# Performance work log

Measured on AMD Instinct MI355X. Metric: run time of the kernel, lower is better.

Reference implementation:

```python
import jax, jax.numpy as jnp
import numpy as np

EPS = 1e-8          # EPSILON in source
THRESH = 0.5        # state.match_threshold
MIN_RADIUS = 0.05   # meaningful-observation threshold

B, T, H, D, N = 4, 4096, 2048, 256, 32768
Hq = H // 4


def setup_inputs() -> dict:
    key = jax.random.key(0)
    ks = jax.random.split(key, 10)
    s = 0.02
    return {
        "hidden": jax.random.normal(ks[0], (B, T, H), jnp.float32),
        "beliefs": jax.random.normal(ks[1], (N, D), jnp.float32),
        "active_mask": jax.random.bernoulli(ks[2], 0.5, (N,)),
        "W_obs": jax.random.normal(ks[3], (D, H), jnp.float32) * s,
        "W_g1": jax.random.normal(ks[4], (Hq, H), jnp.float32) * s,
        "b_g1": jnp.zeros((Hq,), jnp.float32),
        "W_g2": jax.random.normal(ks[5], (1, Hq), jnp.float32) * s,
        "b_g2": jnp.full((1,), -2.0, jnp.float32),  # nn.init.constant_(bias, -2.0)
        "W_p1": jax.random.normal(ks[6], (Hq, H), jnp.float32) * s,
        "b_p1": jnp.zeros((Hq,), jnp.float32),
        "W_p2": jax.random.normal(ks[7], (1, Hq), jnp.float32) * s,
        "b_p2": jnp.zeros((1,), jnp.float32),
    }


def reference(hidden, beliefs, active_mask, W_obs, W_g1, b_g1, W_g2, b_g2,
              W_p1, b_p1, W_p2, b_p2):
    # --- projections (torch Linear: y = x @ W.T + b) ---
    obs = jnp.einsum("bth,dh->btd", hidden, W_obs)                       # [B,T,D]
    gate = jax.nn.sigmoid(
        jnp.einsum("btq,oq->bto",
                   jax.nn.relu(jnp.einsum("bth,qh->btq", hidden, W_g1) + b_g1),
                   W_g2) + b_g2)                                          # [B,T,1]
    prec = jax.nn.softplus(
        jnp.einsum("btq,oq->bto",
                   jax.nn.relu(jnp.einsum("bth,qh->btq", hidden, W_p1) + b_p1),
                   W_p2) + b_p2)                                          # [B,T,1]
    gated_prec = gate * prec

    obs_mean = obs.mean(axis=0)          # [T,D]
    prec_mean = gated_prec.mean(axis=0)  # [T,1]
    # F.normalize: x / max(||x||, eps)
    obs_angles = obs_mean / jnp.maximum(
        jnp.linalg.norm(obs_mean, axis=-1, keepdims=True), EPS)
    obs_beliefs = obs_angles * prec_mean  # [T,D] radius = precision

    # --- cosine-similarity 1-NN match against active beliefs ---
    b_radii = jnp.clip(jnp.linalg.norm(beliefs, axis=-1), EPS, None)     # [N]
    b_angles = beliefs / b_radii[:, None]
    o_radii_c = jnp.clip(jnp.linalg.norm(obs_beliefs, axis=-1), EPS, None)
    o_angles = obs_beliefs / o_radii_c[:, None]
    sims = jnp.einsum("td,nd->tn", o_angles, b_angles)                    # [T,N]
    sims_masked = jnp.where(active_mask[None, :], sims, -jnp.inf)
    any_active = jnp.any(active_mask)
    best_sims = jnp.where(any_active, jnp.max(sims_masked, axis=-1), 0.0)  # [T]
    best_global = jnp.where(any_active, jnp.argmax(sims_masked, axis=-1), -1)

    obs_radii = jnp.linalg.norm(obs_beliefs, axis=-1)  # unclamped
    meaningful = obs_radii > MIN_RADIUS
    matched = meaningful & (best_sims > THRESH) & any_active
    slots = jnp.where(matched, best_global, -1)          # matched slot or -1 (new)
    sims_out = jnp.where(matched, best_sims, 0.0)
    return obs_beliefs, sims_out, slots, meaningful
```

## Files before the change

kernel.cpp:

```cpp
#include <hip/hip_runtime.h>
#include <hip/hip_bf16.h>
#include <math.h>

#define TB 4
#define TT 4096
#define HH 2048
#define DD 256
#define NN 32768
#define HQ 512
#define MM (TB*TT)

typedef __attribute__((ext_vector_type(8))) short bf16x8;
typedef __attribute__((ext_vector_type(8))) _Float16 f16x8;
typedef __attribute__((ext_vector_type(4))) float f32x4;

__device__ inline unsigned short f2bf(float x){
  __hip_bfloat16 h = __float2bfloat16(x);
  return *reinterpret_cast<unsigned short*>(&h);
}

__device__ inline unsigned short f2h(float x){
  _Float16 h = (_Float16)x;
  unsigned short u; __builtin_memcpy(&u, &h, 2); return u;
}

__device__ inline bf16x8 as_bf16x8(uint4 u){ bf16x8 r; __builtin_memcpy(&r,&u,16); return r; }

__device__ __forceinline__ void gload_ldsv(const void* g, void* l){
  __builtin_amdgcn_global_load_lds(
      (const __attribute__((address_space(1))) unsigned int*)g,
      (__attribute__((address_space(3))) unsigned int*)l, 16, 0, 0);
}

#define PREP_MEAN 8192
#define PREP_CVTW 1024
#define PREP_WOBS 512
#define PREP_BEL  8192
#define PREP_ZERO 129
#define PREP_GRID (PREP_MEAN+PREP_CVTW+PREP_WOBS+PREP_BEL+PREP_ZERO)
__global__ __launch_bounds__(256) void k_prep(
    const float* __restrict__ h, unsigned short* __restrict__ hmb,
    const float* __restrict__ Wg1, const float* __restrict__ Wp1,
    unsigned short* __restrict__ Wsw,
    const float* __restrict__ Wobs, unsigned short* __restrict__ wob,
    const float* __restrict__ bel, unsigned short* __restrict__ bbf,
    unsigned int* __restrict__ zbase){
  const int b = blockIdx.x;
  if (b < PREP_MEAN){
    const size_t i = (size_t)b*256 + threadIdx.x;
    const size_t TH4 = (size_t)TT*HH/4;
    const float4* p = (const float4*)h;
    float4 v0 = p[i], v1 = p[i+TH4], v2 = p[i+2*TH4], v3 = p[i+3*TH4];
    float4 m;
    m.x = 0.25f*(v0.x+v1.x+v2.x+v3.x);
    m.y = 0.25f*(v0.y+v1.y+v2.y+v3.y);
    m.z = 0.25f*(v0.z+v1.z+v2.z+v3.z);
    m.w = 0.25f*(v0.w+v1.w+v2.w+v3.w);
    ushort4 o; o.x = f2bf(m.x); o.y = f2bf(m.y); o.z = f2bf(m.z); o.w = f2bf(m.w);
    *(ushort4*)(hmb + i*4) = o;
  } else if (b < PREP_MEAN + PREP_CVTW){
    const int id = (b - PREP_MEAN)*256 + threadIdx.x;
    const int n = id >> 8;
    const int cg = id & 255;
    const int k = cg*8;
    const int kc = cg >> 2;
    const int c8 = cg & 3;
    const float* src = (n < HQ) ? (Wg1 + (size_t)n*HH + k) : (Wp1 + (size_t)(n-HQ)*HH + k);
    float4 v0 = *(const float4*)src;
    float4 v1 = *(const float4*)(src + 4);
    unsigned short o[8] = {f2h(v0.x),f2h(v0.y),f2h(v0.z),f2h(v0.w),
                           f2h(v1.x),f2h(v1.y),f2h(v1.z),f2h(v1.w)};
    const int nb = n >> 8, r = n & 255;
    const int s = (r & 3) ^ ((r >> 2) & 3);
    unsigned short* dst = Wsw + ((size_t)(nb*64 + kc))*8192 + r*32 + ((c8 ^ s) << 3);
    __builtin_memcpy(dst, o, 16);
  } else if (b < PREP_MEAN + PREP_CVTW + PREP_WOBS){
    const int idx4 = (b - PREP_MEAN - PREP_CVTW)*256 + threadIdx.x;
    float4 v = *(const float4*)(Wobs + (size_t)idx4*4);
    ushort4 o; o.x = f2bf(v.x); o.y = f2bf(v.y); o.z = f2bf(v.z); o.w = f2bf(v.w);
    *(ushort4*)(wob + (size_t)idx4*4) = o;
  } else if (b < PREP_MEAN + PREP_CVTW + PREP_WOBS + PREP_BEL){
    const int bb = b - (PREP_MEAN + PREP_CVTW + PREP_WOBS);
    const int n = (bb*256 + threadIdx.x) >> 6;
    const int lane = threadIdx.x & 63;
    const float4 v = *(const float4*)(bel + (size_t)n*DD + lane*4);
    float s = v.x*v.x + v.y*v.y + v.z*v.z + v.w*v.w;
    #pragma unroll
    for (int m = 1; m < 64; m <<= 1) s += __shfl_xor(s, m);
    const float inv = 1.f / fmaxf(sqrtf(s), 1e-8f);
    ushort4 o;
    o.x = f2bf(v.x*inv); o.y = f2bf(v.y*inv); o.z = f2bf(v.z*inv); o.w = f2bf(v.w*inv);
    *(ushort4*)(bbf + (size_t)n*DD + lane*4) = o;
  } else {
    const int idx = (b - (PREP_MEAN + PREP_CVTW + PREP_WOBS + PREP_BEL))*256 + threadIdx.x;
    if (idx < 32832) zbase[idx] = 0;
  }
}

__global__ __launch_bounds__(256) void k_obs(const unsigned short* __restrict__ A,
    const unsigned short* __restrict__ Bw,
    const float* __restrict__ z1, const float* __restrict__ z2,
    const float* __restrict__ bg2, const float* __restrict__ bp2,
    float* __restrict__ out0, float* __restrict__ out3,
    unsigned short* __restrict__ obf,
    const unsigned char* __restrict__ mask, int* __restrict__ flag){
  const int blk = blockIdx.x;
  const int tid = threadIdx.x;
  if (blk >= 64){
    const int i = (blk - 64)*256 + tid;
    const int any = (mask[i] != 0) ? 1 : 0;
    if (__ballot(any)){
      if ((tid & 63) == 0) atomicOr(flag, 1);
    }
    return;
  }
  const int m0 = blk*64;
  const int w = tid>>6, lane = tid&63, lr = lane&15, q = lane>>4;
  __shared__ __align__(16) unsigned short As[2][64*32];
  __shared__ __align__(16) unsigned short Bs[2][256*32];
  f32x4 acc[16] = {};
  const int srow = lane >> 2, sch = (lane & 3) ^ (srow & 3);
  const unsigned short* asrc = A + (size_t)(m0 + w*16 + srow)*HH + sch*8;

  gload_ldsv(asrc, &As[0][w*16*32]);
  #pragma unroll
  for (int i = 0; i < 4; i++){
    const unsigned short* bsrc = Bw + (size_t)((i*4 + w)*16 + srow)*HH + sch*8;
    gload_ldsv(bsrc, &Bs[0][(i*4 + w)*16*32]);
  }
  __syncthreads();
  const int px = (q ^ (lr & 3)) << 3;
  for (int t = 0; t < 64; t++){
    const int cur = t & 1;
    if (t < 63){
      const int ko = (t+1)*32;
      gload_ldsv(asrc + ko, &As[cur^1][w*16*32]);
      #pragma unroll
      for (int i = 0; i < 4; i++){
        const unsigned short* bsrc = Bw + (size_t)((i*4 + w)*16 + srow)*HH + ko + sch*8;
        gload_ldsv(bsrc, &Bs[cur^1][(i*4 + w)*16*32]);
      }
    }
    bf16x8 a = as_bf16x8(*(const uint4*)&As[cur][(w*16 + lr)*32 + px]);
    #pragma unroll
    for (int j = 0; j < 16; j++){
      bf16x8 bb = as_bf16x8(*(const uint4*)&Bs[cur][(j*16 + lr)*32 + px]);
      acc[j] = __builtin_amdgcn_mfma_f32_16x16x32_bf16(a, bb, acc[j], 0, 0, 0);
    }
    __syncthreads();
  }
  #pragma unroll
  for (int r = 0; r < 4; r++){
    const int t = m0 + w*16 + q*4 + r;
    float s2 = 0.f;
    #pragma unroll
    for (int j = 0; j < 16; j++) s2 += acc[j][r]*acc[j][r];
    #pragma unroll
    for (int mk = 1; mk < 16; mk <<= 1) s2 += __shfl_xor(s2, mk);
    const float nrm = sqrtf(s2);
    float p = 0.f;
    #pragma unroll
    for (int bb = 0; bb < TB; bb++){
      float a = z1[bb*TT + t] + bg2[0];
      float c = z2[bb*TT + t] + bp2[0];
      float gate = 1.f/(1.f + expf(-a));
      float sp = (c > 0.f) ? (c + log1pf(expf(-c))) : log1pf(expf(c));
      p += gate * sp;
    }
    const float pm = p * 0.25f;
    const float sc = pm / fmaxf(nrm, 1e-8f);
    float qq = 0.f;
    #pragma unroll
    for (int j = 0; j < 16; j++){
      float o = acc[j][r] * sc;
      out0[(size_t)t*DD + j*16 + lr] = o;
      qq += o*o;
    }
    #pragma unroll
    for (int mk = 1; mk < 16; mk <<= 1) qq += __shfl_xor(qq, mk);
    const float r2 = sqrtf(qq);
    const float inv2 = 1.f / fmaxf(r2, 1e-8f);
    #pragma unroll
    for (int j = 0; j < 16; j++){
      float o = acc[j][r] * sc;
      obf[(size_t)t*DD + j*16 + lr] = f2bf(o * inv2);
    }
    if (lr == 0) out3[t] = (r2 > 0.05f) ? 1.f : 0.f;
  }
}

__global__ __launch_bounds__(512, 2) void k_gp(const float* __restrict__ A,
    const unsigned short* __restrict__ Wsw,
    const float* __restrict__ bg1, const float* __restrict__ bp1,
    const float* __restrict__ Wg2, const float* __restrict__ Wp2,
    float* __restrict__ z1, float* __restrict__ z2){
  const int bid = blockIdx.x;
  const int s5 = bid >> 3;
  const int nb = s5 & 3;
  const int my = ((s5 >> 2) << 3) | (bid & 7);
  const int m0 = my*256;
  const int tid = threadIdx.x;
  const int w = tid>>6, lane = tid&63, lr = lane&15, q = lane>>4;
  __shared__ __align__(16) unsigned short Ws[2][8192];
  __shared__ __align__(16) float As[2][8192];
  f32x4 acc[2][16] = {};

  const unsigned short* wtp = Wsw + (size_t)nb*64*8192 + w*1024 + lane*8;
  const int rpB = lr*32 + ((q ^ ((lr & 3) ^ ((lr >> 2) & 3))) << 3);
  const int sr8 = lane >> 3;
  const int sc  = (lane & 7) ^ sr8;
  const float* asrc = A + (size_t)(m0 + w*32 + sr8)*HH + sc*4;

  #pragma unroll
  for (int i = 0; i < 4; i++) gload_ldsv(asrc + (size_t)i*8*HH, &As[0][(w*32 + i*8)*32]);
  #pragma unroll
  for (int i = 0; i < 2; i++) gload_ldsv(wtp + i*512, &Ws[0][w*1024 + i*512]);
  __syncthreads();

  for (int t = 0; t < 64; t++){
    const int cur = t & 1;
    if (t < 63){
      #pragma unroll
      for (int i = 0; i < 4; i++)
        gload_ldsv(asrc + (size_t)i*8*HH + (t+1)*32, &As[cur^1][(w*32 + i*8)*32]);
      #pragma unroll
      for (int i = 0; i < 2; i++)
        gload_ldsv(wtp + (size_t)(t+1)*8192 + i*512, &Ws[cur^1][w*1024 + i*512]);
    }
    const float* At = As[cur];
    f16x8 ah[2], al[2];
    #pragma unroll
    for (int i = 0; i < 2; i++){
      const int tr = w*32 + i*16 + lr;
      const int pxx = lr & 7;
      float4 fa = *(const float4*)&At[tr*32 + (((2*q)   ^ pxx) << 2)];
      float4 fb = *(const float4*)&At[tr*32 + (((2*q+1) ^ pxx) << 2)];
      float av[8] = {fa.x,fa.y,fa.z,fa.w, fb.x,fb.y,fb.z,fb.w};
      #pragma unroll
      for (int e = 0; e < 8; e++){
        _Float16 h = (_Float16)av[e];
        ah[i][e] = h; al[i][e] = (_Float16)(av[e] - (float)h);
      }
    }
    const unsigned short* Wc = Ws[cur];
    __builtin_amdgcn_s_setprio(1);
    #pragma unroll
    for (int jp = 0; jp < 8; jp++){
      f16x8 b0, b1;
      __builtin_memcpy(&b0, Wc + (2*jp)*512 + rpB, 16);
      __builtin_memcpy(&b1, Wc + (2*jp+1)*512 + rpB, 16);
      acc[0][2*jp]   = __builtin_amdgcn_mfma_f32_16x16x32_f16(ah[0], b0, acc[0][2*jp],   0, 0, 0);
      acc[1][2*jp]   = __builtin_amdgcn_mfma_f32_16x16x32_f16(ah[1], b0, acc[1][2*jp],   0, 0, 0);
      acc[0][2*jp+1] = __builtin_amdgcn_mfma_f32_16x16x32_f16(ah[0], b1, acc[0][2*jp+1], 0, 0, 0);
      acc[1][2*jp+1] = __builtin_amdgcn_mfma_f32_16x16x32_f16(ah[1], b1, acc[1][2*jp+1], 0, 0, 0);
      acc[0][2*jp]   = __builtin_amdgcn_mfma_f32_16x16x32_f16(al[0], b0, acc[0][2*jp],   0, 0, 0);
      acc[1][2*jp]   = __builtin_amdgcn_mfma_f32_16x16x32_f16(al[1], b0, acc[1][2*jp],   0, 0, 0);
      acc[0][2*jp+1] = __builtin_amdgcn_mfma_f32_16x16x32_f16(al[0], b1, acc[0][2*jp+1], 0, 0, 0);
      acc[1][2*jp+1] = __builtin_amdgcn_mfma_f32_16x16x32_f16(al[1], b1, acc[1][2*jp+1], 0, 0, 0);
    }
    __builtin_amdgcn_s_setprio(0);
    __syncthreads();
  }

  const bool isP = (nb >= 2);
  const float* b1p = isP ? bp1 : bg1;
  const float* w2 = isP ? Wp2 : Wg2;
  float* zt = isP ? z2 : z1;
  const int nbl = nb*256 - (isP ? HQ : 0);
  float s[2][4] = {};
  #pragma unroll
  for (int j = 0; j < 16; j++){
    const int n = nbl + j*16 + lr;
    const float bb = b1p[n], ww = w2[n];
    #pragma unroll
    for (int i = 0; i < 2; i++)
      #pragma unroll
      for (int r = 0; r < 4; r++)
        s[i][r] += fmaxf(acc[i][j][r] + bb, 0.f) * ww;
  }
  #pragma unroll
  for (int mk = 1; mk < 16; mk <<= 1)
    #pragma unroll
    for (int i = 0; i < 2; i++)
      #pragma unroll
      for (int r = 0; r < 4; r++)
        s[i][r] += __shfl_xor(s[i][r], mk);
  if (lr == 0){
    #pragma unroll
    for (int i = 0; i < 2; i++)
      #pragma unroll
      for (int r = 0; r < 4; r++)
        atomicAdd(&zt[m0 + w*32 + i*16 + q*4 + r], s[i][r]);
  }
}

__global__ __launch_bounds__(256) void k_sims(const unsigned short* __restrict__ obf,
    const unsigned short* __restrict__ bbf, const unsigned char* __restrict__ mask,
    float* __restrict__ pmax, int* __restrict__ pidx){
  const int bid = blockIdx.x;
  const int u = bid >> 3;
  const int ns = (bid & 7) + ((u >> 4) << 3);
  const int t0 = (u & 15) * 256;
  const int nbase0 = ns * (NN/32);
  const int tid = threadIdx.x;
  const int w = tid >> 6, lane = tid & 63;
  const int lr = lane & 15, q = lane >> 4;
  __shared__ __align__(16) unsigned short bt[2][32*256];
  __shared__ __align__(16) unsigned char am[1024];
  const int srow = lane >> 5;
  const int sp   = lane & 31;

  ((unsigned int*)am)[tid] = ((const unsigned int*)(mask + nbase0))[tid];

  #pragma unroll
  for (int i = 0; i < 4; i++){
    const int row = (i*4 + w)*2 + srow;
    const unsigned short* src = bbf + (size_t)(nbase0 + row)*DD + ((sp ^ (row & 31)) << 3);
    gload_ldsv(src, &bt[0][(i*4 + w)*512]);
  }
  bf16x8 afr[4][8];
  #pragma unroll
  for (int i = 0; i < 4; i++){
    const unsigned short* ap = obf + (size_t)(t0 + w*64 + i*16 + lr)*DD + q*8;
    #pragma unroll
    for (int ks = 0; ks < 8; ks++)
      afr[i][ks] = as_bf16x8(*(const uint4*)(ap + ks*32));
  }
  __syncthreads();

  float vmax[4][4]; int vidx[4][4];
  #pragma unroll
  for (int i = 0; i < 4; i++)
    #pragma unroll
    for (int r = 0; r < 4; r++){ vmax[i][r] = -INFINITY; vidx[i][r] = -1; }

  int cur = 0;
  for (int it = 0; it < 32; it++){
    const int nl = it*32;
    if (it < 31){
      #pragma unroll
      for (int i = 0; i < 4; i++){
        const int row = (i*4 + w)*2 + srow;
        const unsigned short* src = bbf + (size_t)(nbase0 + nl + 32 + row)*DD + ((sp ^ (row & 31)) << 3);
        gload_ldsv(src, &bt[cur^1][(i*4 + w)*512]);
      }
    }
    const unsigned short* btc = bt[cur];
    #pragma unroll
    for (int sub = 0; sub < 2; sub++){
      const int rowi = sub*16 + lr;
      const bool act = (am[nl + rowi] != 0);
      const unsigned short* bp = btc + rowi*256;
      f32x4 acc[4] = {};
      __builtin_amdgcn_s_setprio(1);
      #pragma unroll
      for (int ks = 0; ks < 8; ks++){
        const int p = (q + ks*4) ^ rowi;
        bf16x8 bfr = as_bf16x8(*(const uint4*)(bp + (p & 31)*8));
        #pragma unroll
        for (int i = 0; i < 4; i++)
          acc[i] = __builtin_amdgcn_mfma_f32_16x16x32_bf16(afr[i][ks], bfr, acc[i], 0, 0, 0);
      }
      __builtin_amdgcn_s_setprio(0);
      if (act){
        const int n = nbase0 + nl + rowi;
        #pragma unroll
        for (int i = 0; i < 4; i++)
          #pragma unroll
          for (int r = 0; r < 4; r++)
            if (acc[i][r] > vmax[i][r]){ vmax[i][r] = acc[i][r]; vidx[i][r] = n; }
      }
    }
    __syncthreads();
    cur ^= 1;
  }
  #pragma unroll
  for (int mk = 1; mk < 16; mk <<= 1){
    #pragma unroll
    for (int i = 0; i < 4; i++)
      #pragma unroll
      for (int r = 0; r < 4; r++){
        float om = __shfl_xor(vmax[i][r], mk);
        int   oi = __shfl_xor(vidx[i][r], mk);
        if (om > vmax[i][r] || (om == vmax[i][r] && (unsigned)oi < (unsigned)vidx[i][r])){
          vmax[i][r] = om; vidx[i][r] = oi;
        }
      }
  }
  if (lr == 0){
    #pragma unroll
    for (int i = 0; i < 4; i++)
      #pragma unroll
      for (int r = 0; r < 4; r++){
        const int t = t0 + w*64 + i*16 + q*4 + r;
        pmax[ns*TT + t] = vmax[i][r];
        pidx[ns*TT + t] = vidx[i][r];
      }
  }
}

__global__ __launch_bounds__(256) void k_combine(const float* __restrict__ pmax,
    const int* __restrict__ pidx, const float* __restrict__ out3,
    const int* __restrict__ flag, float* __restrict__ out1, float* __restrict__ out2){
  const int t = blockIdx.x*256 + threadIdx.x;
  float best = -INFINITY; int bi = -1;
  #pragma unroll
  for (int s = 0; s < 32; s++){
    float m = pmax[s*TT + t];
    if (m > best){ best = m; bi = pidx[s*TT + t]; }
  }
  const bool anyA = (flag[0] != 0);
  const bool mf = out3[t] != 0.f;
  const bool matched = mf && anyA && (best > 0.5f);
  out1[t] = matched ? best : 0.f;
  out2[t] = matched ? (float)bi : -1.f;
}

extern "C" void kernel_launch(void* const* d_in, const int* in_sizes, int n_in,
                              void* d_out, int out_size, void* d_ws, size_t ws_size,
                              hipStream_t stream) {
  const float* hidden = (const float*)d_in[0];
  const float* beliefs = (const float*)d_in[1];
  const unsigned char* amask = (const unsigned char*)d_in[2];
  const float* W_obs = (const float*)d_in[3];
  const float* W_g1 = (const float*)d_in[4];
  const float* b_g1 = (const float*)d_in[5];
  const float* W_g2 = (const float*)d_in[6];
  const float* b_g2 = (const float*)d_in[7];
  const float* W_p1 = (const float*)d_in[8];
  const float* b_p1 = (const float*)d_in[9];
  const float* W_p2 = (const float*)d_in[10];
  const float* b_p2 = (const float*)d_in[11];

  char* ws = (char*)d_ws;
  const size_t HMB_OFF  = 0;
  const size_t WSW_OFF  = 16777216;
  const size_t WOB_OFF  = 20971520;
  const size_t Z1_OFF   = 26214400;
  const size_t Z2_OFF   = 26279936;
  const size_t FLAG_OFF = 26345472;
  const size_t OBF_OFF  = 26362112;
  const size_t BBF_OFF  = 28459264;
  const size_t PMAX_OFF = 45236480;
  const size_t PIDX_OFF = 45760768;

  unsigned short* hmb = (unsigned short*)(ws + HMB_OFF);
  unsigned short* Wsw = (unsigned short*)(ws + WSW_OFF);
  unsigned short* wob = (unsigned short*)(ws + WOB_OFF);
  float* z1  = (float*)(ws + Z1_OFF);
  float* z2  = (float*)(ws + Z2_OFF);
  int*   flg = (int*)(ws + FLAG_OFF);
  unsigned short* obf = (unsigned short*)(ws + OBF_OFF);
  unsigned short* bbf = (unsigned short*)(ws + BBF_OFF);
  float* pmax = (float*)(ws + PMAX_OFF);
  int*   pidx = (int*)(ws + PIDX_OFF);

  float* out0 = (float*)d_out;
  float* out1 = out0 + (size_t)TT*DD;
  float* out2 = out1 + TT;
  float* out3 = out2 + TT;

  k_prep    <<<PREP_GRID, 256, 0, stream>>>(hidden, hmb, W_g1, W_p1, Wsw,
                W_obs, wob, beliefs, bbf, (unsigned int*)z1);
  k_gp      <<<256, 512, 0, stream>>>(hidden, Wsw, b_g1, b_p1, W_g2, W_p2, z1, z2);
  k_obs     <<<64 + NN/256, 256, 0, stream>>>(hmb, wob, z1, z2, b_g2, b_p2,
                out0, out3, obf, amask, flg);
  k_sims    <<<512, 256, 0, stream>>>(obf, bbf, amask, pmax, pidx);
  k_combine <<<TT/256, 256, 0, stream>>>(pmax, pidx, out3, flg, out1, out2);
}
```

Measured before the change: 524.4 us.

## Split obs GEMM over K with atomics, retile gate GEMM, add finalize kernel

The observation projection GEMM, previously only 64 blocks over the full K, is split four ways along K into 256 blocks that atomically add fp32 partials into a zeroed buffer. A separate finalize kernel then computes precision, normalization, output writes and the bf16 angles. The gate/precision GEMM is retiled from 512-thread blocks with 256 rows to 256-thread blocks with 128 rows, doubling the grid. This aims to fill more CUs during the small GEMM, at the cost of extra atomic traffic, a zeroing pass and one more kernel launch.

```diff
diff --git a/kernel.cpp b/kernel.cpp
--- a/kernel.cpp
+++ b/kernel.cpp
@@ -37,14 +37,15 @@
 #define PREP_WOBS 512
 #define PREP_BEL  8192
 #define PREP_ZERO 129
-#define PREP_GRID (PREP_MEAN+PREP_CVTW+PREP_WOBS+PREP_BEL+PREP_ZERO)
+#define PREP_ZOM  1024
+#define PREP_GRID (PREP_MEAN+PREP_CVTW+PREP_WOBS+PREP_BEL+PREP_ZERO+PREP_ZOM)
 __global__ __launch_bounds__(256) void k_prep(
     const float* __restrict__ h, unsigned short* __restrict__ hmb,
     const float* __restrict__ Wg1, const float* __restrict__ Wp1,
     unsigned short* __restrict__ Wsw,
     const float* __restrict__ Wobs, unsigned short* __restrict__ wob,
     const float* __restrict__ bel, unsigned short* __restrict__ bbf,
-    unsigned int* __restrict__ zbase){
+    unsigned int* __restrict__ zbase, float* __restrict__ om){
   const int b = blockIdx.x;
   if (b < PREP_MEAN){
     const size_t i = (size_t)b*256 + threadIdx.x;
@@ -91,53 +92,46 @@
     ushort4 o;
     o.x = f2bf(v.x*inv); o.y = f2bf(v.y*inv); o.z = f2bf(v.z*inv); o.w = f2bf(v.w*inv);
     *(ushort4*)(bbf + (size_t)n*DD + lane*4) = o;
-  } else {
+  } else if (b < PREP_MEAN + PREP_CVTW + PREP_WOBS + PREP_BEL + PREP_ZERO){
     const int idx = (b - (PREP_MEAN + PREP_CVTW + PREP_WOBS + PREP_BEL))*256 + threadIdx.x;
     if (idx < 32832) zbase[idx] = 0;
-  }
-}
-
-__global__ __launch_bounds__(256) void k_obs(const unsigned short* __restrict__ A,
-    const unsigned short* __restrict__ Bw,
-    const float* __restrict__ z1, const float* __restrict__ z2,
-    const float* __restrict__ bg2, const float* __restrict__ bp2,
-    float* __restrict__ out0, float* __restrict__ out3,
-    unsigned short* __restrict__ obf,
-    const unsigned char* __restrict__ mask, int* __restrict__ flag){
-  const int blk = blockIdx.x;
+  } else {
+    const int idx = (b - (PREP_MEAN + PREP_CVTW + PREP_WOBS + PREP_BEL + PREP_ZERO))*256
+                    + threadIdx.x;
+    float4 z = {0.f, 0.f, 0.f, 0.f};
+    *(float4*)(om + (size_t)idx*4) = z;
+  }
+}
+
+__global__ __launch_bounds__(256) void k_obsp(const unsigned short* __restrict__ A,
+    const unsigned short* __restrict__ Bw, float* __restrict__ om){
+  const int bid = blockIdx.x;
+  const int m0 = (bid & 63) * 64;
+  const int k0 = (bid >> 6) * 512;
   const int tid = threadIdx.x;
-  if (blk >= 64){
-    const int i = (blk - 64)*256 + tid;
-    const int any = (mask[i] != 0) ? 1 : 0;
-    if (__ballot(any)){
-      if ((tid & 63) == 0) atomicOr(flag, 1);
-    }
-    return;
-  }
-  const int m0 = blk*64;
   const int w = tid>>6, lane = tid&63, lr = lane&15, q = lane>>4;
   __shared__ __align__(16) unsigned short As[2][64*32];
   __shared__ __align__(16) unsigned short Bs[2][256*32];
   f32x4 acc[16] = {};
   const int srow = lane >> 2, sch = (lane & 3) ^ (srow & 3);
-  const unsigned short* asrc = A + (size_t)(m0 + w*16 + srow)*HH + sch*8;
+  const unsigned short* asrc = A + (size_t)(m0 + w*16 + srow)*HH + k0 + sch*8;
 
   gload_ldsv(asrc, &As[0][w*16*32]);
   #pragma unroll
   for (int i = 0; i < 4; i++){
-    const unsigned short* bsrc = Bw + (size_t)((i*4 + w)*16 + srow)*HH + sch*8;
+    const unsigned short* bsrc = Bw + (size_t)((i*4 + w)*16 + srow)*HH + k0 + sch*8;
     gload_ldsv(bsrc, &Bs[0][(i*4 + w)*16*32]);
   }
   __syncthreads();
   const int px = (q ^ (lr & 3)) << 3;
-  for (int t = 0; t < 64; t++){
+  for (int t = 0; t < 16; t++){
     const int cur = t & 1;
-    if (t < 63){
+    if (t < 15){
       const int ko = (t+1)*32;
       gload_ldsv(asrc + ko, &As[cur^1][w*16*32]);
       #pragma unroll
       for (int i = 0; i < 4; i++){
-        const unsigned short* bsrc = Bw + (size_t)((i*4 + w)*16 + srow)*HH + ko + sch*8;
+        const unsigned short* bsrc = Bw + (size_t)((i*4 + w)*16 + srow)*HH + k0 + ko + sch*8;
         gload_ldsv(bsrc, &Bs[cur^1][(i*4 + w)*16*32]);
       }
     }
@@ -150,62 +144,28 @@
     __syncthreads();
   }
   #pragma unroll
-  for (int r = 0; r < 4; r++){
-    const int t = m0 + w*16 + q*4 + r;
-    float s2 = 0.f;
-    #pragma unroll
-    for (int j = 0; j < 16; j++) s2 += acc[j][r]*acc[j][r];
-    #pragma unroll
-    for (int mk = 1; mk < 16; mk <<= 1) s2 += __shfl_xor(s2, mk);
-    const float nrm = sqrtf(s2);
-    float p = 0.f;
-    #pragma unroll
-    for (int bb = 0; bb < TB; bb++){
-      float a = z1[bb*TT + t] + bg2[0];
-      float c = z2[bb*TT + t] + bp2[0];
-      float gate = 1.f/(1.f + expf(-a));
-      float sp = (c > 0.f) ? (c + log1pf(expf(-c))) : log1pf(expf(c));
-      p += gate * sp;
-    }
-    const float pm = p * 0.25f;
-    const float sc = pm / fmaxf(nrm, 1e-8f);
-    float qq = 0.f;
-    #pragma unroll
-    for (int j = 0; j < 16; j++){
-      float o = acc[j][r] * sc;
-      out0[(size_t)t*DD + j*16 + lr] = o;
-      qq += o*o;
-    }
-    #pragma unroll
-    for (int mk = 1; mk < 16; mk <<= 1) qq += __shfl_xor(qq, mk);
-    const float r2 = sqrtf(qq);
-    const float inv2 = 1.f / fmaxf(r2, 1e-8f);
-    #pragma unroll
-    for (int j = 0; j < 16; j++){
-      float o = acc[j][r] * sc;
-      obf[(size_t)t*DD + j*16 + lr] = f2bf(o * inv2);
-    }
-    if (lr == 0) out3[t] = (r2 > 0.05f) ? 1.f : 0.f;
-  }
-}
-
-__global__ __launch_bounds__(512, 2) void k_gp(const float* __restrict__ A,
+  for (int j = 0; j < 16; j++)
+    #pragma unroll
+    for (int r = 0; r < 4; r++)
+      atomicAdd(&om[(size_t)(m0 + w*16 + q*4 + r)*DD + j*16 + lr], acc[j][r]);
+}
+
+__global__ __launch_bounds__(256, 2) void k_gp(const float* __restrict__ A,
     const unsigned short* __restrict__ Wsw,
     const float* __restrict__ bg1, const float* __restrict__ bp1,
     const float* __restrict__ Wg2, const float* __restrict__ Wp2,
     float* __restrict__ z1, float* __restrict__ z2){
   const int bid = blockIdx.x;
-  const int s5 = bid >> 3;
-  const int nb = s5 & 3;
-  const int my = ((s5 >> 2) << 3) | (bid & 7);
-  const int m0 = my*256;
+  const int nb = (bid >> 3) & 3;
+  const int my = (bid & 7) + ((bid >> 5) << 3);
+  const int m0 = my*128;
   const int tid = threadIdx.x;
   const int w = tid>>6, lane = tid&63, lr = lane&15, q = lane>>4;
   __shared__ __align__(16) unsigned short Ws[2][8192];
-  __shared__ __align__(16) float As[2][8192];
+  __shared__ __align__(16) float As[2][4096];
   f32x4 acc[2][16] = {};
 
-  const unsigned short* wtp = Wsw + (size_t)nb*64*8192 + w*1024 + lane*8;
+  const unsigned short* wt = Wsw + (size_t)nb*64*8192 + w*2048 + lane*8;
   const int rpB = lr*32 + ((q ^ ((lr & 3) ^ ((lr >> 2) & 3))) << 3);
   const int sr8 = lane >> 3;
   const int sc  = (lane & 7) ^ sr8;
@@ -214,7 +174,7 @@
   #pragma unroll
   for (int i = 0; i < 4; i++) gload_ldsv(asrc + (size_t)i*8*HH, &As[0][(w*32 + i*8)*32]);
   #pragma unroll
-  for (int i = 0; i < 2; i++) gload_ldsv(wtp + i*512, &Ws[0][w*1024 + i*512]);
+  for (int i = 0; i < 4; i++) gload_ldsv(wt + i*512, &Ws[0][w*2048 + i*512]);
   __syncthreads();
 
   for (int t = 0; t < 64; t++){
@@ -224,8 +184,8 @@
       for (int i = 0; i < 4; i++)
         gload_ldsv(asrc + (size_t)i*8*HH + (t+1)*32, &As[cur^1][(w*32 + i*8)*32]);
       #pragma unroll
-      for (int i = 0; i < 2; i++)
-        gload_ldsv(wtp + (size_t)(t+1)*8192 + i*512, &Ws[cur^1][w*1024 + i*512]);
+      for (int i = 0; i < 4; i++)
+        gload_ldsv(wt + (size_t)(t+1)*8192 + i*512, &Ws[cur^1][w*2048 + i*512]);
     }
     const float* At = As[cur];
     f16x8 ah[2], al[2];
@@ -292,6 +252,53 @@
       for (int r = 0; r < 4; r++)
         atomicAdd(&zt[m0 + w*32 + i*16 + q*4 + r], s[i][r]);
   }
+}
+
+__global__ __launch_bounds__(256) void k_fin(const float* __restrict__ om,
+    const float* __restrict__ z1, const float* __restrict__ z2,
+    const float* __restrict__ bg2, const float* __restrict__ bp2,
+    float* __restrict__ out0, float* __restrict__ out3,
+    unsigned short* __restrict__ obf,
+    const unsigned char* __restrict__ mask, int* __restrict__ flag){
+  const int blk = blockIdx.x;
+  const int tid = threadIdx.x;
+  if (blk >= 1024){
+    const int i = (blk - 1024)*256 + tid;
+    const int any = (mask[i] != 0) ? 1 : 0;
+    if (__ballot(any)){
+      if ((tid & 63) == 0) atomicOr(flag, 1);
+    }
+    return;
+  }
+  const int w = tid >> 6, lane = tid & 63;
+  const int t = blk*4 + w;
+  float pm = 0.f;
+  if (lane < TB){
+    float a = z1[lane*TT + t] + bg2[0];
+    float b = z2[lane*TT + t] + bp2[0];
+    float gate = 1.f/(1.f + expf(-a));
+    float sp = (b > 0.f) ? (b + log1pf(expf(-b))) : log1pf(expf(b));
+    pm = gate * sp;
+  }
+  #pragma unroll
+  for (int m = 1; m < 4; m <<= 1) pm += __shfl_xor(pm, m);
+  pm = __shfl(pm, 0) * 0.25f;
+  float4 x = *(const float4*)(om + (size_t)t*DD + lane*4);
+  float ss = x.x*x.x + x.y*x.y + x.z*x.z + x.w*x.w;
+  #pragma unroll
+  for (int m = 1; m < 64; m <<= 1) ss += __shfl_xor(ss, m);
+  const float nrm = sqrtf(ss);
+  const float sc = pm / fmaxf(nrm, 1e-8f);
+  float4 ob = {x.x*sc, x.y*sc, x.z*sc, x.w*sc};
+  *(float4*)(out0 + (size_t)t*DD + lane*4) = ob;
+  float s2 = ob.x*ob.x + ob.y*ob.y + ob.z*ob.z + ob.w*ob.w;
+  #pragma unroll
+  for (int m = 1; m < 64; m <<= 1) s2 += __shfl_xor(s2, m);
+  const float r2 = sqrtf(s2);
+  if (lane == 0) out3[t] = (r2 > 0.05f) ? 1.f : 0.f;
+  const float inv2 = 1.f / fmaxf(r2, 1e-8f);
+  ushort4 o = {f2bf(ob.x*inv2), f2bf(ob.y*inv2), f2bf(ob.z*inv2), f2bf(ob.w*inv2)};
+  *(ushort4*)(obf + (size_t)t*DD + lane*4) = o;
 }
 
 __global__ __launch_bounds__(256) void k_sims(const unsigned short* __restrict__ obf,
@@ -436,6 +443,7 @@
   const size_t HMB_OFF  = 0;
   const size_t WSW_OFF  = 16777216;
   const size_t WOB_OFF  = 20971520;
+  const size_t OM_OFF   = 22020096;
   const size_t Z1_OFF   = 26214400;
   const size_t Z2_OFF   = 26279936;
   const size_t FLAG_OFF = 26345472;
@@ -447,6 +455,7 @@
   unsigned short* hmb = (unsigned short*)(ws + HMB_OFF);
   unsigned short* Wsw = (unsigned short*)(ws + WSW_OFF);
   unsigned short* wob = (unsigned short*)(ws + WOB_OFF);
+  float* om  = (float*)(ws + OM_OFF);
   float* z1  = (float*)(ws + Z1_OFF);
   float* z2  = (float*)(ws + Z2_OFF);
   int*   flg = (int*)(ws + FLAG_OFF);
@@ -461,9 +470,10 @@
   float* out3 = out2 + TT;
 
   k_prep    <<<PREP_GRID, 256, 0, stream>>>(hidden, hmb, W_g1, W_p1, Wsw,
-                W_obs, wob, beliefs, bbf, (unsigned int*)z1);
-  k_gp      <<<256, 512, 0, stream>>>(hidden, Wsw, b_g1, b_p1, W_g2, W_p2, z1, z2);
-  k_obs     <<<64 + NN/256, 256, 0, stream>>>(hmb, wob, z1, z2, b_g2, b_p2,
+                W_obs, wob, beliefs, bbf, (unsigned int*)z1, om);
+  k_obsp    <<<256, 256, 0, stream>>>(hmb, wob, om);
+  k_gp      <<<512, 256, 0, stream>>>(hidden, Wsw, b_g1, b_p1, W_g2, W_p2, z1, z2);
+  k_fin     <<<1024 + NN/256, 256, 0, stream>>>(om, z1, z2, b_g2, b_p2,
                 out0, out3, obf, amask, flg);
   k_sims    <<<512, 256, 0, stream>>>(obf, bbf, amask, pmax, pidx);
   k_combine <<<TT/256, 256, 0, stream>>>(pmax, pidx, out3, flg, out1, out2);
```

Result: faster. 461.5 us (-12.0%).
